# Kernel optimization log

Hardware: AMD Instinct MI355X
Metric: run time of the kernel (lower is better)

## Reference

```python
import jax, jax.numpy as jnp
import numpy as np

DIM = 128
N_NODES = 100000
N_EDGES = 200000
M = 800000  # incidence pairs in each direction
L = 2
N_CLASS = 10


def setup_inputs() -> dict:
    key = jax.random.key(0)
    ks = jax.random.split(key, 8)
    s = 1.0 / np.sqrt(DIM)
    return {
        "node_x": jax.random.normal(ks[0], (N_NODES, DIM), jnp.float32),
        "nodes_map": jax.random.randint(ks[1], (M,), 0, N_NODES, jnp.int32),
        "edge_seg": jnp.sort(jax.random.randint(ks[2], (M,), 0, N_EDGES, jnp.int32)),
        "edges_map": jax.random.randint(ks[3], (M,), 0, N_EDGES, jnp.int32),
        "node_seg": jnp.sort(jax.random.randint(ks[4], (M,), 0, N_NODES, jnp.int32)),
        "num_edges": N_EDGES,
        "W_e": jax.random.normal(ks[5], (L, DIM, DIM), jnp.float32) * s,
        "b_e": jnp.zeros((L, DIM), jnp.float32),
        "g_e": jnp.ones((L, DIM), jnp.float32),
        "be_e": jnp.zeros((L, DIM), jnp.float32),
        "W_n": jax.random.normal(ks[6], (L, DIM, DIM), jnp.float32) * s,
        "b_n": jnp.zeros((L, DIM), jnp.float32),
        "g_n": jnp.ones((L, DIM), jnp.float32),
        "be_n": jnp.zeros((L, DIM), jnp.float32),
        "W_c": jax.random.normal(ks[7], (DIM, N_CLASS), jnp.float32) * s,
        "b_c": jnp.zeros((N_CLASS,), jnp.float32),
    }


def _seg_mean(x, seg, num_segments):
    # global_mean_pool: segment sum / count (count clamped to 1 for empty segments)
    s = jax.ops.segment_sum(x, seg, num_segments=num_segments)
    cnt = jax.ops.segment_sum(jnp.ones((x.shape[0],), x.dtype), seg, num_segments=num_segments)
    return s / jnp.maximum(cnt, 1.0)[:, None]


def _layernorm(x, g, b, eps=1e-5):
    m = jnp.mean(x, axis=-1, keepdims=True)
    v = jnp.mean(jnp.square(x - m), axis=-1, keepdims=True)
    return (x - m) * jax.lax.rsqrt(v + eps) * g + b


def reference(node_x, nodes_map, edge_seg, edges_map, node_seg, num_edges,
              W_e, b_e, g_e, be_e, W_n, b_n, g_n, be_n, W_c, b_c):
    n_nodes = node_x.shape[0]
    x = node_x  # in_drp = Dropout(0.0) is identity
    for i in range(W_e.shape[0]):
        # N2E: gather node feats per (edge, member) pair, mean-pool per hyperedge
        ex = _seg_mean(x[nodes_map], edge_seg, num_edges)          # [E, DIM]
        ex = jax.nn.relu(_layernorm(ex @ W_e[i] + b_e[i], g_e[i], be_e[i]))
        # E2N: gather edge feats per (node, incident-edge) pair, mean-pool per node
        x = _seg_mean(ex[edges_map], node_seg, n_nodes)            # [N, DIM]
        x = jax.nn.relu(_layernorm(x @ W_n[i] + b_n[i], g_n[i], be_n[i]))
    return jax.nn.log_softmax(x @ W_c + b_c, axis=-1)
```

## Files before the change

kernel.cpp:

```cpp
#include <hip/hip_runtime.h>
#include <hip/hip_bf16.h>

#define DIM 128

typedef __bf16 bf16x8 __attribute__((ext_vector_type(8)));
typedef float f32x4 __attribute__((ext_vector_type(4)));

static inline int cdiv(int a, int b) { return (a + b - 1) / b; }
static inline size_t align256(size_t x) { return (x + 255) & ~size_t(255); }

__device__ inline unsigned short f2bf(float f) {
    union { float f; unsigned int u; } v; v.f = f;
    unsigned int r = v.u + 0x7fff + ((v.u >> 16) & 1);
    return (unsigned short)(r >> 16);
}
__device__ inline unsigned int hb(float f) {
    return (__builtin_bit_cast(unsigned int, f) + 0x8000u) >> 16;
}

__global__ void seg_offsets_kernel(const int* __restrict__ seg, int m, int nseg,
                                   int* __restrict__ off) {
    int s = blockIdx.x * blockDim.x + threadIdx.x;
    if (s > nseg) return;
    int lo = 0, hi = m;
    while (lo < hi) {
        int mid = (lo + hi) >> 1;
        if (seg[mid] < s) lo = mid + 1; else hi = mid;
    }
    off[s] = lo;
}

__global__ void f32_to_bf16_kernel(const float* __restrict__ in,
                                   unsigned short* __restrict__ out, int n4) {
    int i = blockIdx.x * blockDim.x + threadIdx.x;
    if (i >= n4) return;
    float4 v = ((const float4*)in)[i];
    ushort4 o;
    o.x = f2bf(v.x); o.y = f2bf(v.y); o.z = f2bf(v.z); o.w = f2bf(v.w);
    ((ushort4*)out)[i] = o;
}

__global__ void swizzle_w_kernel(const float* __restrict__ W_e, const float* __restrict__ W_n,
                                 unsigned short* __restrict__ wsw) {
    int gid = blockIdx.x * blockDim.x + threadIdx.x;
    int mi = gid >> 11;
    int e = gid & 2047;
    const float* W = (mi < 2) ? (W_e + (size_t)mi * DIM * DIM)
                              : (W_n + (size_t)(mi - 2) * DIM * DIM);
    int t = e >> 9, n = (e >> 6) & 7, lane = e & 63;
    int q = lane >> 4, c = lane & 15;
    int k0 = t * 32 + q * 8, col = n * 16 + c;
    unsigned short vals[8];
#pragma unroll
    for (int j = 0; j < 8; ++j) vals[j] = f2bf(W[(size_t)(k0 + j) * DIM + col]);
    ushort4* dst = (ushort4*)(wsw + (size_t)gid * 8);
    dst[0] = make_ushort4(vals[0], vals[1], vals[2], vals[3]);
    dst[1] = make_ushort4(vals[4], vals[5], vals[6], vals[7]);
}

__device__ inline void accum8s(float* a, uint4 v, float wt) {
    unsigned int u[4] = {v.x, v.y, v.z, v.w};
#pragma unroll
    for (int i = 0; i < 4; ++i) {
        float lo = __builtin_bit_cast(float, u[i] << 16);
        float hi = __builtin_bit_cast(float, u[i]);
        a[2 * i]     = fmaf(wt, lo, a[2 * i]);
        a[2 * i + 1] = fmaf(wt, hi, a[2 * i + 1]);
    }
}

__global__ __launch_bounds__(256)
void fused_pool_gemm_ln_relu_v3_kernel(const uint4* __restrict__ src,
                                       const int* __restrict__ map,
                                       const int* __restrict__ off,
                                       const unsigned short* __restrict__ Wsw,
                                       const float* __restrict__ b,
                                       const float* __restrict__ g,
                                       const float* __restrict__ be,
                                       unsigned short* __restrict__ Y,
                                       int nseg) {
    __shared__ unsigned short alds[64][136];
    int tid = threadIdx.x;
    int w = tid >> 6, lane = tid & 63;
    int q = lane >> 4, c = lane & 15;
    int blockbase = blockIdx.x * 64;
    int wavebase = w * 16;

    float bcol[8], gcol[8], becol[8];
#pragma unroll
    for (int n = 0; n < 8; ++n) {
        int col = n * 16 + c;
        bcol[n] = b[col]; gcol[n] = g[col]; becol[n] = be[col];
    }

    int begv[4], endv[4];
#pragma unroll
    for (int it = 0; it < 4; ++it) {
        int sc = min(blockbase + wavebase + it * 4 + q, nseg - 1);
        begv[it] = off[sc];
        endv[it] = off[sc + 1];
    }

    for (int it = 0; it < 4; ++it) {
        int s_local = wavebase + it * 4 + q;
        int beg = begv[it], end = endv[it];
        float a[8] = {0.f, 0.f, 0.f, 0.f, 0.f, 0.f, 0.f, 0.f};
        for (int j = beg; j < end; j += 4) {
            int j1 = min(j + 1, end - 1), j2 = min(j + 2, end - 1), j3 = min(j + 3, end - 1);
            int r0 = map[j], r1 = map[j1], r2 = map[j2], r3 = map[j3];
            uint4 v0 = src[(size_t)r0 * 16 + c];
            uint4 v1 = src[(size_t)r1 * 16 + c];
            uint4 v2 = src[(size_t)r2 * 16 + c];
            uint4 v3 = src[(size_t)r3 * 16 + c];
            accum8s(a, v0, 1.f);
            accum8s(a, v1, (j + 1 < end) ? 1.f : 0.f);
            accum8s(a, v2, (j + 2 < end) ? 1.f : 0.f);
            accum8s(a, v3, (j + 3 < end) ? 1.f : 0.f);
        }
        float inv = 1.f / fmaxf((float)(end - beg), 1.f);
        uint4 o;
        o.x = hb(a[0] * inv) | (hb(a[1] * inv) << 16);
        o.y = hb(a[2] * inv) | (hb(a[3] * inv) << 16);
        o.z = hb(a[4] * inv) | (hb(a[5] * inv) << 16);
        o.w = hb(a[6] * inv) | (hb(a[7] * inv) << 16);
        *(uint4*)&alds[s_local][c * 8] = o;
    }

    f32x4 acc[8];
#pragma unroll
    for (int n = 0; n < 8; ++n) acc[n] = f32x4{bcol[n], bcol[n], bcol[n], bcol[n]};

    const bf16x8* ap = (const bf16x8*)&alds[wavebase + c][q * 8];
    bf16x8 afr[4] = {ap[0], ap[4], ap[8], ap[12]};

    const bf16x8* wg = (const bf16x8*)Wsw;
    bf16x8 wcur[8], wnxt[8];
#pragma unroll
    for (int n = 0; n < 8; ++n) wcur[n] = wg[n * 64 + lane];
#pragma unroll
    for (int t = 0; t < 4; ++t) {
        if (t < 3) {
#pragma unroll
            for (int n = 0; n < 8; ++n) wnxt[n] = wg[((t + 1) * 8 + n) * 64 + lane];
        }
#pragma unroll
        for (int n = 0; n < 8; ++n)
            acc[n] = __builtin_amdgcn_mfma_f32_16x16x32_bf16(afr[t], wcur[n], acc[n], 0, 0, 0);
#pragma unroll
        for (int n = 0; n < 8; ++n) wcur[n] = wnxt[n];
    }

    float s1[4], s2[4];
#pragma unroll
    for (int j = 0; j < 4; ++j) {
        float t1 = 0.f, t2 = 0.f;
#pragma unroll
        for (int n = 0; n < 8; ++n) { float v = acc[n][j]; t1 += v; t2 = fmaf(v, v, t2); }
        s1[j] = t1; s2[j] = t2;
    }
#pragma unroll
    for (int o = 1; o < 16; o <<= 1)
#pragma unroll
        for (int j = 0; j < 4; ++j) {
            s1[j] += __shfl_xor(s1[j], o);
            s2[j] += __shfl_xor(s2[j], o);
        }

#pragma unroll
    for (int j = 0; j < 4; ++j) {
        int row = blockbase + wavebase + q * 4 + j;
        if (row >= nseg) continue;
        float m = s1[j] * (1.f / DIM);
        float var = fmaf(-m, m, s2[j] * (1.f / DIM));
        float inv = rsqrtf(var + 1e-5f);
        unsigned short* yp = Y + (size_t)row * DIM + c;
#pragma unroll
        for (int n = 0; n < 8; ++n) {
            float d = acc[n][j] - m;
            float y = fmaxf(fmaf(d * inv, gcol[n], becol[n]), 0.f);
            unsigned int u = __builtin_bit_cast(unsigned int, y) + 0x8000u;
            yp[n * 16] = (unsigned short)(u >> 16);
        }
    }
}

#define CL_ROWS 4
__global__ __launch_bounds__(256)
void classifier_logsoftmax_v3_kernel(const uint4* __restrict__ X,
                                     const float* __restrict__ Wc,
                                     const float* __restrict__ bc,
                                     float* __restrict__ out, int nrows) {
    int w = threadIdx.x >> 6, lane = threadIdx.x & 63;
    int g = lane >> 4, c16 = lane & 15;
    int r0 = (blockIdx.x * 16 + w * 4 + g) * CL_ROWS;
    if (r0 >= nrows) return;

    float wc[8][10];
#pragma unroll
    for (int j = 0; j < 8; ++j)
#pragma unroll
        for (int c = 0; c < 10; ++c) wc[j][c] = Wc[(c16 * 8 + j) * 10 + c];
    float bcv[10];
#pragma unroll
    for (int c = 0; c < 10; ++c) bcv[c] = bc[c];

    int rend = min(r0 + CL_ROWS, nrows);
    for (int r = r0; r < rend; ++r) {
        uint4 v = X[(size_t)r * 16 + c16];
        float x[8];
        {
            unsigned int u[4] = {v.x, v.y, v.z, v.w};
#pragma unroll
            for (int i = 0; i < 4; ++i) {
                union { unsigned int ui; float f; } lo, hi;
                lo.ui = u[i] << 16;
                hi.ui = u[i] & 0xffff0000u;
                x[2 * i] = lo.f; x[2 * i + 1] = hi.f;
            }
        }
        float acc[10];
#pragma unroll
        for (int c = 0; c < 10; ++c) acc[c] = 0.f;
#pragma unroll
        for (int j = 0; j < 8; ++j)
#pragma unroll
            for (int c = 0; c < 10; ++c) acc[c] = fmaf(x[j], wc[j][c], acc[c]);

#pragma unroll
        for (int o = 1; o < 16; o <<= 1)
#pragma unroll
            for (int c = 0; c < 10; ++c) acc[c] += __shfl_xor(acc[c], o);

#pragma unroll
        for (int c = 0; c < 10; ++c) acc[c] += bcv[c];

        float mx = acc[0];
#pragma unroll
        for (int c = 1; c < 10; ++c) mx = fmaxf(mx, acc[c]);
        float se = 0.f;
#pragma unroll
        for (int c = 0; c < 10; ++c) se += expf(acc[c] - mx);
        float lse = mx + logf(se);

        float myv = 0.f;
#pragma unroll
        for (int c = 0; c < 10; ++c) myv = (c16 == c) ? acc[c] : myv;
        if (c16 < 10) out[(size_t)r * 10 + c16] = myv - lse;
    }
}

extern "C" void kernel_launch(void* const* d_in, const int* in_sizes, int n_in,
                              void* d_out, int out_size, void* d_ws, size_t ws_size,
                              hipStream_t stream) {
    const float* node_x    = (const float*)d_in[0];
    const int*   nodes_map = (const int*)d_in[1];
    const int*   edge_seg  = (const int*)d_in[2];
    const int*   edges_map = (const int*)d_in[3];
    const int*   node_seg  = (const int*)d_in[4];
    const float* W_e = (const float*)d_in[6];
    const float* b_e = (const float*)d_in[7];
    const float* g_e = (const float*)d_in[8];
    const float* be_e= (const float*)d_in[9];
    const float* W_n = (const float*)d_in[10];
    const float* b_n = (const float*)d_in[11];
    const float* g_n = (const float*)d_in[12];
    const float* be_n= (const float*)d_in[13];
    const float* W_c = (const float*)d_in[14];
    const float* b_c = (const float*)d_in[15];
    float* out = (float*)d_out;

    const int N = in_sizes[0] / DIM;
    const int M = in_sizes[1];
    const int E = 200000;
    const int L = in_sizes[6] / (DIM * DIM);

    char* ws = (char*)d_ws;
    int* edge_off = (int*)ws;           ws += align256((size_t)(E + 1) * sizeof(int));
    int* node_off = (int*)ws;           ws += align256((size_t)(N + 1) * sizeof(int));
    unsigned short* wsw = (unsigned short*)ws;      ws += align256((size_t)4 * 2048 * 8 * sizeof(unsigned short));
    unsigned short* node_xb = (unsigned short*)ws;  ws += align256((size_t)N * DIM * sizeof(unsigned short));
    unsigned short* exb = (unsigned short*)ws;      ws += align256((size_t)E * DIM * sizeof(unsigned short));
    unsigned short* xb  = (unsigned short*)ws;      ws += align256((size_t)N * DIM * sizeof(unsigned short));
    (void)ws_size;

    seg_offsets_kernel<<<cdiv(E + 1, 256), 256, 0, stream>>>(edge_seg, M, E, edge_off);
    seg_offsets_kernel<<<cdiv(N + 1, 256), 256, 0, stream>>>(node_seg, M, N, node_off);
    f32_to_bf16_kernel<<<cdiv(N * DIM / 4, 256), 256, 0, stream>>>(node_x, node_xb, N * DIM / 4);
    swizzle_w_kernel<<<32, 256, 0, stream>>>(W_e, W_n, wsw);

    const unsigned short* xcur = node_xb;
    for (int i = 0; i < L; ++i) {
        fused_pool_gemm_ln_relu_v3_kernel<<<cdiv(E, 64), 256, 0, stream>>>(
            (const uint4*)xcur, nodes_map, edge_off, wsw + (size_t)i * 16384,
            b_e + i * DIM, g_e + i * DIM, be_e + i * DIM, exb, E);
        fused_pool_gemm_ln_relu_v3_kernel<<<cdiv(N, 64), 256, 0, stream>>>(
            (const uint4*)exb, edges_map, node_off, wsw + (size_t)(2 + i) * 16384,
            b_n + i * DIM, g_n + i * DIM, be_n + i * DIM, xb, N);
        xcur = xb;
    }

    classifier_logsoftmax_v3_kernel<<<cdiv(N, 16 * CL_ROWS), 256, 0, stream>>>(
        (const uint4*)xcur, W_c, b_c, out, N);
}
```

Baseline: 365.0 us.

## Stage weights in LDS, double block size, swizzle A tile, use 32-bit gather addressing

Each block now has 512 threads covering 128 segments and first copies the full swizzled 128x128 bf16 weight matrix into shared memory. The MFMA loop then reads weights from LDS instead of having every wave fetch them from global memory. The A tile drops its padded layout for an XOR swizzle that avoids bank conflicts, and gather addresses use 32-bit shift arithmetic. The cost is a 32 KB weight load plus a barrier per block and about 64 KB of LDS per block, which may lower occupancy; the 32-bit offsets assume the source tensor is under 4 GB.

```diff
diff --git a/kernel.cpp b/kernel.cpp
--- a/kernel.cpp
+++ b/kernel.cpp
@@ -69,8 +69,8 @@
     }
 }
 
-__global__ __launch_bounds__(256)
-void fused_pool_gemm_ln_relu_v3_kernel(const uint4* __restrict__ src,
+__global__ __launch_bounds__(512)
+void fused_pool_gemm_ln_relu_v5_kernel(const uint4* __restrict__ src,
                                        const int* __restrict__ map,
                                        const int* __restrict__ off,
                                        const unsigned short* __restrict__ Wsw,
@@ -79,11 +79,20 @@
                                        const float* __restrict__ be,
                                        unsigned short* __restrict__ Y,
                                        int nseg) {
-    __shared__ unsigned short alds[64][136];
+    __shared__ bf16x8 wlds[2048];
+    __shared__ unsigned short alds[128 * 128];
     int tid = threadIdx.x;
     int w = tid >> 6, lane = tid & 63;
     int q = lane >> 4, c = lane & 15;
-    int blockbase = blockIdx.x * 64;
+
+    {
+        const uint4* gsrc = (const uint4*)Wsw;
+        uint4* ldst = (uint4*)wlds;
+#pragma unroll
+        for (int i = 0; i < 4; ++i) ldst[tid + i * 512] = gsrc[tid + i * 512];
+    }
+
+    int blockbase = blockIdx.x * 128;
     int wavebase = w * 16;
 
     float bcol[8], gcol[8], becol[8];
@@ -92,7 +101,6 @@
         int col = n * 16 + c;
         bcol[n] = b[col]; gcol[n] = g[col]; becol[n] = be[col];
     }
-
     int begv[4], endv[4];
 #pragma unroll
     for (int it = 0; it < 4; ++it) {
@@ -101,17 +109,22 @@
         endv[it] = off[sc + 1];
     }
 
+    __syncthreads();
+
+    const char* sbase = (const char*)src;
+    unsigned cb = (unsigned)(c << 4);
     for (int it = 0; it < 4; ++it) {
         int s_local = wavebase + it * 4 + q;
         int beg = begv[it], end = endv[it];
         float a[8] = {0.f, 0.f, 0.f, 0.f, 0.f, 0.f, 0.f, 0.f};
         for (int j = beg; j < end; j += 4) {
             int j1 = min(j + 1, end - 1), j2 = min(j + 2, end - 1), j3 = min(j + 3, end - 1);
-            int r0 = map[j], r1 = map[j1], r2 = map[j2], r3 = map[j3];
-            uint4 v0 = src[(size_t)r0 * 16 + c];
-            uint4 v1 = src[(size_t)r1 * 16 + c];
-            uint4 v2 = src[(size_t)r2 * 16 + c];
-            uint4 v3 = src[(size_t)r3 * 16 + c];
+            unsigned r0 = (unsigned)map[j], r1 = (unsigned)map[j1];
+            unsigned r2 = (unsigned)map[j2], r3 = (unsigned)map[j3];
+            uint4 v0 = *(const uint4*)(sbase + ((r0 << 8) + cb));
+            uint4 v1 = *(const uint4*)(sbase + ((r1 << 8) + cb));
+            uint4 v2 = *(const uint4*)(sbase + ((r2 << 8) + cb));
+            uint4 v3 = *(const uint4*)(sbase + ((r3 << 8) + cb));
             accum8s(a, v0, 1.f);
             accum8s(a, v1, (j + 1 < end) ? 1.f : 0.f);
             accum8s(a, v2, (j + 2 < end) ? 1.f : 0.f);
@@ -123,31 +136,27 @@
         o.y = hb(a[2] * inv) | (hb(a[3] * inv) << 16);
         o.z = hb(a[4] * inv) | (hb(a[5] * inv) << 16);
         o.w = hb(a[6] * inv) | (hb(a[7] * inv) << 16);
-        *(uint4*)&alds[s_local][c * 8] = o;
+        uint4* wrow = (uint4*)(alds + (size_t)s_local * 128);
+        wrow[c ^ (s_local & 7)] = o;
     }
 
     f32x4 acc[8];
 #pragma unroll
     for (int n = 0; n < 8; ++n) acc[n] = f32x4{bcol[n], bcol[n], bcol[n], bcol[n]};
 
-    const bf16x8* ap = (const bf16x8*)&alds[wavebase + c][q * 8];
-    bf16x8 afr[4] = {ap[0], ap[4], ap[8], ap[12]};
-
-    const bf16x8* wg = (const bf16x8*)Wsw;
-    bf16x8 wcur[8], wnxt[8];
-#pragma unroll
-    for (int n = 0; n < 8; ++n) wcur[n] = wg[n * 64 + lane];
-#pragma unroll
-    for (int t = 0; t < 4; ++t) {
-        if (t < 3) {
-#pragma unroll
-            for (int n = 0; n < 8; ++n) wnxt[n] = wg[((t + 1) * 8 + n) * 64 + lane];
-        }
-#pragma unroll
-        for (int n = 0; n < 8; ++n)
-            acc[n] = __builtin_amdgcn_mfma_f32_16x16x32_bf16(afr[t], wcur[n], acc[n], 0, 0, 0);
-#pragma unroll
-        for (int n = 0; n < 8; ++n) wcur[n] = wnxt[n];
+    const uint4* arow = (const uint4*)(alds + (size_t)(wavebase + c) * 128);
+    int key = c & 7;
+    bf16x8 a0 = *(const bf16x8*)&arow[(q + 0) ^ key];
+    bf16x8 a1 = *(const bf16x8*)&arow[(q + 4) ^ key];
+    bf16x8 a2 = *(const bf16x8*)&arow[(q + 8) ^ key];
+    bf16x8 a3 = *(const bf16x8*)&arow[(q + 12) ^ key];
+
+#pragma unroll
+    for (int n = 0; n < 8; ++n) {
+        acc[n] = __builtin_amdgcn_mfma_f32_16x16x32_bf16(a0, wlds[(0 * 8 + n) * 64 + lane], acc[n], 0, 0, 0);
+        acc[n] = __builtin_amdgcn_mfma_f32_16x16x32_bf16(a1, wlds[(1 * 8 + n) * 64 + lane], acc[n], 0, 0, 0);
+        acc[n] = __builtin_amdgcn_mfma_f32_16x16x32_bf16(a2, wlds[(2 * 8 + n) * 64 + lane], acc[n], 0, 0, 0);
+        acc[n] = __builtin_amdgcn_mfma_f32_16x16x32_bf16(a3, wlds[(3 * 8 + n) * 64 + lane], acc[n], 0, 0, 0);
     }
 
     float s1[4], s2[4];
@@ -290,10 +299,10 @@
 
     const unsigned short* xcur = node_xb;
     for (int i = 0; i < L; ++i) {
-        fused_pool_gemm_ln_relu_v3_kernel<<<cdiv(E, 64), 256, 0, stream>>>(
+        fused_pool_gemm_ln_relu_v5_kernel<<<cdiv(E, 128), 512, 0, stream>>>(
             (const uint4*)xcur, nodes_map, edge_off, wsw + (size_t)i * 16384,
             b_e + i * DIM, g_e + i * DIM, be_e + i * DIM, exb, E);
-        fused_pool_gemm_ln_relu_v3_kernel<<<cdiv(N, 64), 256, 0, stream>>>(
+        fused_pool_gemm_ln_relu_v5_kernel<<<cdiv(N, 128), 512, 0, stream>>>(
             (const uint4*)exb, edges_map, node_off, wsw + (size_t)(2 + i) * 16384,
             b_n + i * DIM, g_n + i * DIM, be_n + i * DIM, xb, N);
         xcur = xb;
```

Result: faster. 349.4 us (-4.3%).
